# Kernel tuning notes

Measured on AMD Instinct MI355X. Metric: run time of the kernel, lower is better.

Reference implementation:

```python
import jax, jax.numpy as jnp
import numpy as np
from jax import lax

B, C, H, W = 4, 3, 512, 512
PATCH = 64
STRIDE = 32
CHANS = [(3, 32), (32, 32), (32, 64), (64, 64), (64, 64), (64, 32), (32, 32), (32, 2)]


def _conv(x, w, b):
    y = lax.conv_general_dilated(x, w, (1, 1), [(1, 1), (1, 1)],
                                 dimension_numbers=('NCHW', 'OIHW', 'NCHW'))
    return y + b[None, :, None, None]


def _pool(x):  # MaxPool2d(2)
    return lax.reduce_window(x, -jnp.inf, lax.max, (1, 1, 2, 2), (1, 1, 2, 2), 'VALID')


def _up(x):  # Upsample(scale=2, bilinear, align_corners=False) == half-pixel resize
    b, c, h, w = x.shape
    return jax.image.resize(x, (b, c, 2 * h, 2 * w), 'bilinear')


def _flow_net(x, ws, bs):
    r = jax.nn.relu
    h = r(_conv(x, ws[0], bs[0]))
    h = r(_conv(h, ws[1], bs[1]))
    h = _pool(h)
    h = r(_conv(h, ws[2], bs[2]))
    h = r(_conv(h, ws[3], bs[3]))
    h = _pool(h)
    h = _up(h)
    h = r(_conv(h, ws[4], bs[4]))
    h = r(_conv(h, ws[5], bs[5]))
    h = _up(h)
    h = r(_conv(h, ws[6], bs[6]))
    return jnp.tanh(_conv(h, ws[7], bs[7]))  # [B,2,H,W]


def _bilinear_zeros(img, gx, gy):
    # img [C,H,W], gx/gy [N,P,P] in [-1,1]; grid_sample bilinear, zeros padding, align_corners=False
    Hh, Ww = img.shape[1], img.shape[2]
    ix = ((gx + 1.0) * Ww - 1.0) * 0.5
    iy = ((gy + 1.0) * Hh - 1.0) * 0.5
    x0 = jnp.floor(ix)
    y0 = jnp.floor(iy)
    wx1 = ix - x0
    wy1 = iy - y0

    def corner(xi, yi, wgt):
        valid = (xi >= 0) & (xi <= Ww - 1) & (yi >= 0) & (yi <= Hh - 1)
        xc = jnp.clip(xi, 0, Ww - 1).astype(jnp.int32)
        yc = jnp.clip(yi, 0, Hh - 1).astype(jnp.int32)
        return img[:, yc, xc] * (wgt * valid)[None]  # [C,N,P,P]

    return (corner(x0, y0, (1 - wx1) * (1 - wy1))
            + corner(x0 + 1, y0, wx1 * (1 - wy1))
            + corner(x0, y0 + 1, (1 - wx1) * wy1)
            + corner(x0 + 1, y0 + 1, wx1 * wy1))


def _forward(x, ws, bs, temp):
    b, c, h, w = x.shape
    flow = _flow_net(x, ws, bs)  # [B,2,H,W]
    gy, gx = jnp.meshgrid(jnp.linspace(-1.0, 1.0, h), jnp.linspace(-1.0, 1.0, w), indexing='ij')
    base = jnp.stack([gx, gy], axis=-1)  # [H,W,2] (x,y)
    deformed = base[None] + flow.transpose(0, 2, 3, 1) * temp  # [B,H,W,2]
    centers = deformed[:, ::STRIDE, ::STRIDE, :].reshape(b, -1, 2)  # [B,N,2]
    py, px = jnp.meshgrid(jnp.linspace(-1.0, 1.0, PATCH), jnp.linspace(-1.0, 1.0, PATCH), indexing='ij')
    pgx = centers[:, :, None, None, 0] + px[None, None] * (PATCH / w)  # [B,N,P,P]
    pgy = centers[:, :, None, None, 1] + py[None, None] * (PATCH / h)
    patches = jax.vmap(_bilinear_zeros)(x, pgx, pgy)  # [B,C,N,P,P]
    patches = patches.transpose(0, 2, 1, 3, 4)  # [B,N,C,P,P]
    return patches, flow, deformed


def setup_inputs() -> dict:
    key = jax.random.key(0)
    ks = jax.random.split(key, len(CHANS) + 1)
    d = {"x": jax.random.normal(ks[0], (B, C, H, W), jnp.float32)}
    for i, (ci, co) in enumerate(CHANS):
        d[f"w{i}"] = jax.random.normal(ks[i + 1], (co, ci, 3, 3), jnp.float32) * 0.01
        d[f"b{i}"] = jnp.zeros((co,), jnp.float32)
    d["temp"] = jnp.full((1,), 0.1, jnp.float32)
    return d


def reference(x, w0, b0, w1, b1, w2, b2, w3, b3, w4, b4, w5, b5, w6, b6, w7, b7, temp):
    ws = [w0, w1, w2, w3, w4, w5, w6, w7]
    bs = [b0, b1, b2, b3, b4, b5, b6, b7]
    return _forward(x, ws, bs, temp)
```

## Files before the change

kernel.cpp:

```cpp
#include <hip/hip_runtime.h>
#include <hip/hip_bf16.h>

typedef __hip_bfloat16 bf16;
typedef unsigned short ushort_t;
typedef __attribute__((ext_vector_type(8))) short short8;
typedef __attribute__((ext_vector_type(4))) float float4v;

#define BATCH 4
#define HH 512
#define WW 512

__device__ __forceinline__ ushort_t f2bfu(float f) {
  __hip_bfloat16 h = __float2bfloat16(f);
  union { __hip_bfloat16 h; ushort_t u; } c;
  c.h = h;
  return c.u;
}
__device__ __forceinline__ float bfu2f(ushort_t u) {
  return __uint_as_float(((unsigned)u) << 16);
}

__device__ __forceinline__ void dma16(void* lds, const void* g) {
  __builtin_amdgcn_global_load_lds(
      (const __attribute__((address_space(1))) unsigned int*)g,
      (__attribute__((address_space(3))) unsigned int*)lds, 16, 0, 0);
}

struct WP { const float* w[8]; };

__global__ __launch_bounds__(256) void prep_w(WP wp, bf16* __restrict__ dst) {
  const int O[8]   = {32, 32, 64, 64, 64, 32, 32, 2};
  const int I[8]   = {3, 32, 32, 64, 64, 64, 32, 32};
  const int OP[8]  = {32, 32, 64, 64, 64, 32, 32, 16};
  const int IP[8]  = {32, 32, 32, 64, 64, 64, 32, 32};
  const int OFF[8] = {0, 9216, 18432, 36864, 73728, 110592, 129024, 138240};
  int l = blockIdx.y;
  int e = blockIdx.x * 256 + threadIdx.x;
  int n = 9 * OP[l] * IP[l];
  if (e >= n) return;
  int tap = e / (OP[l] * IP[l]);
  int rem = e - tap * OP[l] * IP[l];
  int o = rem / IP[l];
  int i = rem - o * IP[l];
  float v = 0.0f;
  if (o < O[l] && i < I[l]) v = wp.w[l][((o * I[l]) + i) * 9 + tap];
  dst[OFF[l] + e] = __float2bfloat16(v);
}

__global__ __launch_bounds__(256) void pack_x(const float* __restrict__ x,
                                              bf16* __restrict__ xp) {
  int i = blockIdx.x * 256 + threadIdx.x;
  if (i >= BATCH * HH * WW) return;
  int b = i / (HH * WW);
  int px = i - b * (HH * WW);
  union { uint4 v; ushort_t s[8]; } o;
  o.v = make_uint4(0, 0, 0, 0);
  const float* p = x + (long)b * 3 * HH * WW + px;
  o.s[0] = f2bfu(p[0]);
  o.s[1] = f2bfu(p[HH * WW]);
  o.s[2] = f2bfu(p[2 * HH * WW]);
  *(uint4*)&xp[(long)i * 8] = o.v;
}

template <int CIN, int COUT, int COUTR, int ACT, int IN_MODE, int OUT_MODE>
__global__ __launch_bounds__(256) void conv_mfma(
    const void* __restrict__ in_, const bf16* __restrict__ wt,
    const float* __restrict__ bias, void* __restrict__ out_, int H, int W,
    const float* __restrict__ temp, float* __restrict__ def) {
  constexpr int MT = COUT / 16;
  constexpr int CK = 32;
  __shared__ alignas(16) bf16 in_lds[324 * CK];
  __shared__ alignas(16) bf16 w_lds[9 * COUT * CK];

  const int tid = threadIdx.x;
  const int lane = tid & 63;
  const int wid = tid >> 6;
  const int lm = lane & 15;
  const int quad = lane >> 4;
  const int x0 = blockIdx.x * 16;
  const int y0 = blockIdx.y * 16;
  const int b = blockIdx.z;

  float4v acc[MT][4];
#pragma unroll
  for (int mt = 0; mt < MT; ++mt) {
    float4v bv;
    if constexpr (COUTR == COUT) {
      bv = *(const float4v*)(bias + mt * 16 + quad * 4);
    } else {
#pragma unroll
      for (int r = 0; r < 4; ++r) {
        int co = mt * 16 + quad * 4 + r;
        bv[r] = (co < COUTR) ? bias[co] : 0.0f;
      }
    }
#pragma unroll
    for (int nt = 0; nt < 4; ++nt) acc[mt][nt] = bv;
  }

  for (int c0 = 0; c0 < CIN; c0 += CK) {
    if constexpr (IN_MODE == 3) {
      const bf16* in = (const bf16*)in_;
      for (int u = tid; u < 324 * 4; u += 256) {
        int px = u >> 2;
        int seg = u & 3;
        int hy = px / 18, hx = px - hy * 18;
        int gy = y0 - 1 + hy, gx = x0 - 1 + hx;
        uint4 v = make_uint4(0, 0, 0, 0);
        if (seg == 0 && gy >= 0 && gy < H && gx >= 0 && gx < W)
          v = *(const uint4*)(in + (((long)b * H + gy) * W + gx) * 8);
        *(uint4*)&in_lds[px * CK + seg * 8] = v;
      }
    } else if constexpr (IN_MODE == 2) {
      const bf16* in = (const bf16*)in_;
      const int Hs = H >> 1, Ws = W >> 1;
      for (int u = tid; u < 324 * 4; u += 256) {
        int px = u >> 2;
        int seg = u & 3;
        int hy = px / 18, hx = px - hy * 18;
        int gy = y0 - 1 + hy, gx = x0 - 1 + hx;
        uint4 o = make_uint4(0, 0, 0, 0);
        if (gy >= 0 && gy < H && gx >= 0 && gx < W) {
          int ys = (gy >> 1) - ((gy & 1) ? 0 : 1);
          int xs = (gx >> 1) - ((gx & 1) ? 0 : 1);
          float wy = (gy & 1) ? 0.25f : 0.75f;
          float wx = (gx & 1) ? 0.25f : 0.75f;
          int y0c = max(ys, 0), y1c = min(ys + 1, Hs - 1);
          int x0c = max(xs, 0), x1c = min(xs + 1, Ws - 1);
          const bf16* p = in + ((long)b * Hs * Ws) * CIN + c0 + seg * 8;
          union { uint4 v; ushort_t s[8]; } a00, a01, a10, a11, r;
          a00.v = *(const uint4*)(p + ((long)y0c * Ws + x0c) * CIN);
          a01.v = *(const uint4*)(p + ((long)y0c * Ws + x1c) * CIN);
          a10.v = *(const uint4*)(p + ((long)y1c * Ws + x0c) * CIN);
          a11.v = *(const uint4*)(p + ((long)y1c * Ws + x1c) * CIN);
#pragma unroll
          for (int j = 0; j < 8; ++j) {
            float f = (1.0f - wy) * ((1.0f - wx) * bfu2f(a00.s[j]) +
                                     wx * bfu2f(a01.s[j])) +
                      wy * ((1.0f - wx) * bfu2f(a10.s[j]) +
                            wx * bfu2f(a11.s[j]));
            r.s[j] = f2bfu(f);
          }
          o = r.v;
        }
        *(uint4*)&in_lds[px * CK + seg * 8] = o;
      }
    } else {
      const bool interior =
          (x0 >= 1) && (x0 + 16 <= W - 1) && (y0 >= 1) && (y0 + 16 <= H - 1);
      const bf16* in = (const bf16*)in_;
      if (interior) {
        for (int r = wid; r < 18; r += 4) {
          int gy = y0 - 1 + r;
          const bf16* gsrc = in + (((long)b * H + gy) * W + x0) * CIN + c0 +
                             (lane >> 2) * CIN + (lane & 3) * 8;
          dma16(&in_lds[(r * 18 + 1) * CK], gsrc);
        }
        if (tid < 144) {
          int r = tid >> 3;
          int side = (tid >> 2) & 1;
          int seg = tid & 3;
          int gx = side ? (x0 + 16) : (x0 - 1);
          int gy = y0 - 1 + r;
          uint4 v = *(const uint4*)(in + (((long)b * H + gy) * W + gx) * CIN +
                                    c0 + seg * 8);
          *(uint4*)&in_lds[(r * 18 + (side ? 17 : 0)) * CK + seg * 8] = v;
        }
      } else {
        for (int u = tid; u < 324 * 4; u += 256) {
          int px = u >> 2;
          int seg = u & 3;
          int hy = px / 18, hx = px - hy * 18;
          int gy = y0 - 1 + hy, gx = x0 - 1 + hx;
          uint4 v = make_uint4(0, 0, 0, 0);
          if (gy >= 0 && gy < H && gx >= 0 && gx < W)
            v = *(const uint4*)(in + (((long)b * H + gy) * W + gx) * CIN + c0 +
                                seg * 8);
          *(uint4*)&in_lds[px * CK + seg * 8] = v;
        }
      }
    }
    {
      constexpr int WUNITS = 9 * COUT * CK / 8;
      for (int u = tid; u < WUNITS; u += 256) {
        int to = u >> 2;
        int seg = u & 3;
        uint4 v = *(const uint4*)(wt + (long)to * CIN + c0 + seg * 8);
        *(uint4*)&w_lds[to * CK + seg * 8] = v;
      }
    }
    __syncthreads();

#pragma unroll
    for (int tap = 0; tap < 9; ++tap) {
      const int r = tap / 3, s = tap - r * 3;
      short8 afrag[MT], bfrag[4];
#pragma unroll
      for (int mt = 0; mt < MT; ++mt)
        afrag[mt] =
            *(const short8*)&w_lds[(tap * COUT + mt * 16 + lm) * CK + quad * 8];
#pragma unroll
      for (int nt = 0; nt < 4; ++nt) {
        int py = 4 * wid + nt;
        bfrag[nt] =
            *(const short8*)&in_lds[((py + r) * 18 + lm + s) * CK + quad * 8];
      }
#pragma unroll
      for (int mt = 0; mt < MT; ++mt)
#pragma unroll
        for (int nt = 0; nt < 4; ++nt)
          acc[mt][nt] = __builtin_amdgcn_mfma_f32_16x16x32_bf16(
              afrag[mt], bfrag[nt], acc[mt][nt], 0, 0, 0);
    }
    __syncthreads();
  }

  if constexpr (OUT_MODE == 3) {
    bf16* out = (bf16*)out_;
    const int Ho = H >> 1, Wo = W >> 1;
#pragma unroll
    for (int mt = 0; mt < MT; ++mt) {
#pragma unroll
      for (int g = 0; g < 2; ++g) {
        float4v m;
#pragma unroll
        for (int r = 0; r < 4; ++r)
          m[r] = fmaxf(fmaxf(acc[mt][2 * g][r], acc[mt][2 * g + 1][r]), 0.0f);
#pragma unroll
        for (int r = 0; r < 4; ++r) m[r] = fmaxf(m[r], __shfl_xor(m[r], 1, 64));
        if ((lm & 1) == 0) {
          int pyo = (y0 >> 1) + 2 * wid + g;
          int pxo = (x0 >> 1) + (lm >> 1);
          union { uint2 v; ushort_t s[4]; } pk;
#pragma unroll
          for (int r = 0; r < 4; ++r) pk.s[r] = f2bfu(m[r]);
          *(uint2*)&out[(((long)b * Ho + pyo) * Wo + pxo) * COUT + mt * 16 +
                        quad * 4] = pk.v;
        }
      }
    }
  } else {
#pragma unroll
    for (int mt = 0; mt < MT; ++mt) {
#pragma unroll
      for (int nt = 0; nt < 4; ++nt) {
        int gy = y0 + 4 * wid + nt;
        int gx = x0 + lm;
        float4v v = acc[mt][nt];
        if constexpr (OUT_MODE == 0) {
          bf16* out = (bf16*)out_;
          union { uint2 v; ushort_t s[4]; } pk;
#pragma unroll
          for (int r = 0; r < 4; ++r) pk.s[r] = f2bfu(fmaxf(v[r], 0.0f));
          *(uint2*)&out[(((long)b * H + gy) * W + gx) * COUT + mt * 16 +
                        quad * 4] = pk.v;
        } else {
          float* out = (float*)out_;
          if (quad == 0) {
            float fx = tanhf(v[0]);
            float fy = tanhf(v[1]);
            out[(((long)b * 2 + 0) * H + gy) * (long)W + gx] = fx;
            out[(((long)b * 2 + 1) * H + gy) * (long)W + gx] = fy;
            float T = temp[0];
            float2 d;
            d.x = -1.0f + gx * (2.0f / 511.0f) + fx * T;
            d.y = -1.0f + gy * (2.0f / 511.0f) + fy * T;
            *(float2*)&def[(((long)b * H + gy) * W + gx) * 2] = d;
          }
        }
      }
    }
  }
}

__global__ __launch_bounds__(256) void patches_k(const float* __restrict__ x,
                                                 const float* __restrict__ def,
                                                 float* __restrict__ out) {
  int i = blockIdx.x * 256 + threadIdx.x;
  int pj = i & 63;
  int t = i >> 6;
  int pi = t & 63;
  t >>= 6;
  int n = t & 255;
  int b = t >> 8;
  if (b >= BATCH) return;
  int hi = n >> 4, wi = n & 15;
  const float* dptr = def + (((long)b * HH + hi * 32) * WW + wi * 32) * 2;
  float cx = dptr[0], cy = dptr[1];
  float pgx = cx + (-1.0f + pj * (2.0f / 63.0f)) * 0.125f;
  float pgy = cy + (-1.0f + pi * (2.0f / 63.0f)) * 0.125f;
  float ix = ((pgx + 1.0f) * 512.0f - 1.0f) * 0.5f;
  float iy = ((pgy + 1.0f) * 512.0f - 1.0f) * 0.5f;
  float fx0 = floorf(ix), fy0 = floorf(iy);
  float wx1 = ix - fx0, wy1 = iy - fy0;
  int x0 = (int)fx0, y0 = (int)fy0;
  int x1 = x0 + 1, y1 = y0 + 1;
  bool vx0 = (x0 >= 0) && (x0 <= 511), vx1 = (x1 >= 0) && (x1 <= 511);
  bool vy0 = (y0 >= 0) && (y0 <= 511), vy1 = (y1 >= 0) && (y1 <= 511);
  int cx0 = min(max(x0, 0), 511), cx1 = min(max(x1, 0), 511);
  int cy0 = min(max(y0, 0), 511), cy1 = min(max(y1, 0), 511);
  float w00 = (1.0f - wx1) * (1.0f - wy1) * ((vx0 && vy0) ? 1.0f : 0.0f);
  float w01 = wx1 * (1.0f - wy1) * ((vx1 && vy0) ? 1.0f : 0.0f);
  float w10 = (1.0f - wx1) * wy1 * ((vx0 && vy1) ? 1.0f : 0.0f);
  float w11 = wx1 * wy1 * ((vx1 && vy1) ? 1.0f : 0.0f);
#pragma unroll
  for (int c = 0; c < 3; ++c) {
    const float* img = x + ((long)b * 3 + c) * (HH * WW);
    float v = img[cy0 * WW + cx0] * w00 + img[cy0 * WW + cx1] * w01 +
              img[cy1 * WW + cx0] * w10 + img[cy1 * WW + cx1] * w11;
    out[(((long)b * 256 + n) * 3 + c) * 4096 + pi * 64 + pj] = v;
  }
}


extern "C" void kernel_launch(void* const* d_in, const int* in_sizes, int n_in,
                              void* d_out, int out_size, void* d_ws,
                              size_t ws_size, hipStream_t stream) {
  const float* x = (const float*)d_in[0];
  WP wp;
  const float* bs[8];
  for (int i = 0; i < 8; ++i) {
    wp.w[i] = (const float*)d_in[1 + 2 * i];
    bs[i] = (const float*)d_in[2 + 2 * i];
  }
  const float* temp = (const float*)d_in[17];

  float* out = (float*)d_out;
  float* flow = out + 12582912;
  float* def = out + 14680064;

  bf16* wT = (bf16*)d_out;
  const int WOFF[8] = {0, 9216, 18432, 36864, 73728, 110592, 129024, 138240};

  const size_t bufElems = (size_t)BATCH * 512 * 512 * 32;
  bf16* A = (bf16*)d_ws;
  bf16* Bf = A + bufElems;
  bf16* xp = Bf + bufElems;

  prep_w<<<dim3(144, 8), 256, 0, stream>>>(wp, wT);
  {
    int total = BATCH * HH * WW;
    pack_x<<<(total + 255) / 256, 256, 0, stream>>>(x, xp);
  }

  dim3 g512(32, 32, BATCH);
  dim3 g256(16, 16, BATCH);
  dim3 g128(8, 8, BATCH);

  conv_mfma<32, 32, 32, 0, 3, 0>
      <<<g512, 256, 0, stream>>>(xp, wT + WOFF[0], bs[0], A, 512, 512, nullptr, nullptr);
  conv_mfma<32, 32, 32, 0, 0, 3>
      <<<g512, 256, 0, stream>>>(A, wT + WOFF[1], bs[1], Bf, 512, 512, nullptr, nullptr);
  conv_mfma<32, 64, 64, 0, 0, 0>
      <<<g256, 256, 0, stream>>>(Bf, wT + WOFF[2], bs[2], A, 256, 256, nullptr, nullptr);
  conv_mfma<64, 64, 64, 0, 0, 3>
      <<<g256, 256, 0, stream>>>(A, wT + WOFF[3], bs[3], Bf, 256, 256, nullptr, nullptr);
  conv_mfma<64, 64, 64, 0, 2, 0>
      <<<g256, 256, 0, stream>>>(Bf, wT + WOFF[4], bs[4], A, 256, 256, nullptr, nullptr);
  conv_mfma<64, 32, 32, 0, 0, 0>
      <<<g256, 256, 0, stream>>>(A, wT + WOFF[5], bs[5], Bf, 256, 256, nullptr, nullptr);
  conv_mfma<32, 32, 32, 0, 2, 0>
      <<<g512, 256, 0, stream>>>(Bf, wT + WOFF[6], bs[6], A, 512, 512, nullptr, nullptr);
  conv_mfma<32, 16, 2, 1, 0, 2>
      <<<g512, 256, 0, stream>>>(A, wT + WOFF[7], bs[7], flow, 512, 512, temp, def);
  {
    int total = BATCH * 256 * 64 * 64;
    patches_k<<<(total + 255) / 256, 256, 0, stream>>>(x, def, out);
  }
}
```

Baseline: 355.5 us.

## Drop LDS weight staging and make conv tile height a template parameter

Removes the shared-memory copy of the weights. Each wave now reads its A fragments straight from global memory, relying on cache hits for the small weight tensor. It also adds an NT template parameter so the 32-channel conv layers use 16x32 output tiles. Taller tiles reuse the halo better and halve the block count. The trade-off is more live accumulator registers and global-latency weight loads inside the MFMA loop, which could lower occupancy or stall the inner loop.

```diff
diff --git a/kernel.cpp b/kernel.cpp
--- a/kernel.cpp
+++ b/kernel.cpp
@@ -62,15 +62,17 @@
   *(uint4*)&xp[(long)i * 8] = o.v;
 }
 
-template <int CIN, int COUT, int COUTR, int ACT, int IN_MODE, int OUT_MODE>
+template <int CIN, int COUT, int COUTR, int NT, int ACT, int IN_MODE,
+          int OUT_MODE>
 __global__ __launch_bounds__(256) void conv_mfma(
     const void* __restrict__ in_, const bf16* __restrict__ wt,
     const float* __restrict__ bias, void* __restrict__ out_, int H, int W,
     const float* __restrict__ temp, float* __restrict__ def) {
   constexpr int MT = COUT / 16;
   constexpr int CK = 32;
-  __shared__ alignas(16) bf16 in_lds[324 * CK];
-  __shared__ alignas(16) bf16 w_lds[9 * COUT * CK];
+  constexpr int TH = 4 * NT;
+  constexpr int HR = TH + 2;
+  __shared__ alignas(16) bf16 in_lds[HR * 18 * CK];
 
   const int tid = threadIdx.x;
   const int lane = tid & 63;
@@ -78,10 +80,10 @@
   const int lm = lane & 15;
   const int quad = lane >> 4;
   const int x0 = blockIdx.x * 16;
-  const int y0 = blockIdx.y * 16;
+  const int y0 = blockIdx.y * TH;
   const int b = blockIdx.z;
 
-  float4v acc[MT][4];
+  float4v acc[MT][NT];
 #pragma unroll
   for (int mt = 0; mt < MT; ++mt) {
     float4v bv;
@@ -95,13 +97,13 @@
       }
     }
 #pragma unroll
-    for (int nt = 0; nt < 4; ++nt) acc[mt][nt] = bv;
+    for (int nt = 0; nt < NT; ++nt) acc[mt][nt] = bv;
   }
 
   for (int c0 = 0; c0 < CIN; c0 += CK) {
     if constexpr (IN_MODE == 3) {
       const bf16* in = (const bf16*)in_;
-      for (int u = tid; u < 324 * 4; u += 256) {
+      for (int u = tid; u < HR * 18 * 4; u += 256) {
         int px = u >> 2;
         int seg = u & 3;
         int hy = px / 18, hx = px - hy * 18;
@@ -114,7 +116,7 @@
     } else if constexpr (IN_MODE == 2) {
       const bf16* in = (const bf16*)in_;
       const int Hs = H >> 1, Ws = W >> 1;
-      for (int u = tid; u < 324 * 4; u += 256) {
+      for (int u = tid; u < HR * 18 * 4; u += 256) {
         int px = u >> 2;
         int seg = u & 3;
         int hy = px / 18, hx = px - hy * 18;
@@ -147,19 +149,19 @@
       }
     } else {
       const bool interior =
-          (x0 >= 1) && (x0 + 16 <= W - 1) && (y0 >= 1) && (y0 + 16 <= H - 1);
+          (x0 >= 1) && (x0 + 16 <= W - 1) && (y0 >= 1) && (y0 + TH <= H - 1);
       const bf16* in = (const bf16*)in_;
       if (interior) {
-        for (int r = wid; r < 18; r += 4) {
+        for (int r = wid; r < HR; r += 4) {
           int gy = y0 - 1 + r;
           const bf16* gsrc = in + (((long)b * H + gy) * W + x0) * CIN + c0 +
                              (lane >> 2) * CIN + (lane & 3) * 8;
           dma16(&in_lds[(r * 18 + 1) * CK], gsrc);
         }
-        if (tid < 144) {
-          int r = tid >> 3;
-          int side = (tid >> 2) & 1;
-          int seg = tid & 3;
+        for (int u = tid; u < 8 * HR; u += 256) {
+          int r = u >> 3;
+          int side = (u >> 2) & 1;
+          int seg = u & 3;
           int gx = side ? (x0 + 16) : (x0 - 1);
           int gy = y0 - 1 + r;
           uint4 v = *(const uint4*)(in + (((long)b * H + gy) * W + gx) * CIN +
@@ -167,7 +169,7 @@
           *(uint4*)&in_lds[(r * 18 + (side ? 17 : 0)) * CK + seg * 8] = v;
         }
       } else {
-        for (int u = tid; u < 324 * 4; u += 256) {
+        for (int u = tid; u < HR * 18 * 4; u += 256) {
           int px = u >> 2;
           int seg = u & 3;
           int hy = px / 18, hx = px - hy * 18;
@@ -180,35 +182,26 @@
         }
       }
     }
-    {
-      constexpr int WUNITS = 9 * COUT * CK / 8;
-      for (int u = tid; u < WUNITS; u += 256) {
-        int to = u >> 2;
-        int seg = u & 3;
-        uint4 v = *(const uint4*)(wt + (long)to * CIN + c0 + seg * 8);
-        *(uint4*)&w_lds[to * CK + seg * 8] = v;
-      }
-    }
     __syncthreads();
 
 #pragma unroll
     for (int tap = 0; tap < 9; ++tap) {
       const int r = tap / 3, s = tap - r * 3;
-      short8 afrag[MT], bfrag[4];
+      short8 afrag[MT], bfrag[NT];
 #pragma unroll
       for (int mt = 0; mt < MT; ++mt)
-        afrag[mt] =
-            *(const short8*)&w_lds[(tap * COUT + mt * 16 + lm) * CK + quad * 8];
-#pragma unroll
-      for (int nt = 0; nt < 4; ++nt) {
-        int py = 4 * wid + nt;
+        afrag[mt] = *(const short8*)&wt[((long)tap * COUT + mt * 16 + lm) * CIN +
+                                        c0 + quad * 8];
+#pragma unroll
+      for (int nt = 0; nt < NT; ++nt) {
+        int py = NT * wid + nt;
         bfrag[nt] =
             *(const short8*)&in_lds[((py + r) * 18 + lm + s) * CK + quad * 8];
       }
 #pragma unroll
       for (int mt = 0; mt < MT; ++mt)
 #pragma unroll
-        for (int nt = 0; nt < 4; ++nt)
+        for (int nt = 0; nt < NT; ++nt)
           acc[mt][nt] = __builtin_amdgcn_mfma_f32_16x16x32_bf16(
               afrag[mt], bfrag[nt], acc[mt][nt], 0, 0, 0);
     }
@@ -221,7 +214,7 @@
 #pragma unroll
     for (int mt = 0; mt < MT; ++mt) {
 #pragma unroll
-      for (int g = 0; g < 2; ++g) {
+      for (int g = 0; g < NT / 2; ++g) {
         float4v m;
 #pragma unroll
         for (int r = 0; r < 4; ++r)
@@ -229,7 +222,7 @@
 #pragma unroll
         for (int r = 0; r < 4; ++r) m[r] = fmaxf(m[r], __shfl_xor(m[r], 1, 64));
         if ((lm & 1) == 0) {
-          int pyo = (y0 >> 1) + 2 * wid + g;
+          int pyo = (y0 >> 1) + (NT / 2) * wid + g;
           int pxo = (x0 >> 1) + (lm >> 1);
           union { uint2 v; ushort_t s[4]; } pk;
 #pragma unroll
@@ -243,8 +236,8 @@
 #pragma unroll
     for (int mt = 0; mt < MT; ++mt) {
 #pragma unroll
-      for (int nt = 0; nt < 4; ++nt) {
-        int gy = y0 + 4 * wid + nt;
+      for (int nt = 0; nt < NT; ++nt) {
+        int gy = y0 + NT * wid + nt;
         int gx = x0 + lm;
         float4v v = acc[mt][nt];
         if constexpr (OUT_MODE == 0) {
@@ -343,26 +336,26 @@
     pack_x<<<(total + 255) / 256, 256, 0, stream>>>(x, xp);
   }
 
-  dim3 g512(32, 32, BATCH);
+  dim3 g512t(32, 16, BATCH);
+  dim3 g256t(16, 8, BATCH);
   dim3 g256(16, 16, BATCH);
-  dim3 g128(8, 8, BATCH);
-
-  conv_mfma<32, 32, 32, 0, 3, 0>
-      <<<g512, 256, 0, stream>>>(xp, wT + WOFF[0], bs[0], A, 512, 512, nullptr, nullptr);
-  conv_mfma<32, 32, 32, 0, 0, 3>
-      <<<g512, 256, 0, stream>>>(A, wT + WOFF[1], bs[1], Bf, 512, 512, nullptr, nullptr);
-  conv_mfma<32, 64, 64, 0, 0, 0>
+
+  conv_mfma<32, 32, 32, 8, 0, 3, 0>
+      <<<g512t, 256, 0, stream>>>(xp, wT + WOFF[0], bs[0], A, 512, 512, nullptr, nullptr);
+  conv_mfma<32, 32, 32, 8, 0, 0, 3>
+      <<<g512t, 256, 0, stream>>>(A, wT + WOFF[1], bs[1], Bf, 512, 512, nullptr, nullptr);
+  conv_mfma<32, 64, 64, 4, 0, 0, 0>
       <<<g256, 256, 0, stream>>>(Bf, wT + WOFF[2], bs[2], A, 256, 256, nullptr, nullptr);
-  conv_mfma<64, 64, 64, 0, 0, 3>
+  conv_mfma<64, 64, 64, 4, 0, 0, 3>
       <<<g256, 256, 0, stream>>>(A, wT + WOFF[3], bs[3], Bf, 256, 256, nullptr, nullptr);
-  conv_mfma<64, 64, 64, 0, 2, 0>
+  conv_mfma<64, 64, 64, 4, 0, 2, 0>
       <<<g256, 256, 0, stream>>>(Bf, wT + WOFF[4], bs[4], A, 256, 256, nullptr, nullptr);
-  conv_mfma<64, 32, 32, 0, 0, 0>
-      <<<g256, 256, 0, stream>>>(A, wT + WOFF[5], bs[5], Bf, 256, 256, nullptr, nullptr);
-  conv_mfma<32, 32, 32, 0, 2, 0>
-      <<<g512, 256, 0, stream>>>(Bf, wT + WOFF[6], bs[6], A, 512, 512, nullptr, nullptr);
-  conv_mfma<32, 16, 2, 1, 0, 2>
-      <<<g512, 256, 0, stream>>>(A, wT + WOFF[7], bs[7], flow, 512, 512, temp, def);
+  conv_mfma<64, 32, 32, 8, 0, 0, 0>
+      <<<g256t, 256, 0, stream>>>(A, wT + WOFF[5], bs[5], Bf, 256, 256, nullptr, nullptr);
+  conv_mfma<32, 32, 32, 8, 0, 2, 0>
+      <<<g512t, 256, 0, stream>>>(Bf, wT + WOFF[6], bs[6], A, 512, 512, nullptr, nullptr);
+  conv_mfma<32, 16, 2, 8, 1, 0, 2>
+      <<<g512t, 256, 0, stream>>>(A, wT + WOFF[7], bs[7], flow, 512, 512, temp, def);
   {
     int total = BATCH * 256 * 64 * 64;
     patches_k<<<(total + 255) / 256, 256, 0, stream>>>(x, def, out);
```

Result: slower. 429.8 us (+20.9%).

## Fold bilinear upsample into conv6 via polyphase weights; keep weights in registers

Applied to the files above, without the earlier changes.

Replaces the upsample-then-3x3-conv at full resolution with a polyphase convolution on the low-resolution input. Per-phase 3x3 weights are precomputed by folding the bilinear 0.75/0.25 interpolation into conv6's weights. The main kernel clamps at the low-res edges, so a separate scalar kernel recomputes the border ring exactly. Single-chunk convolutions (CIN=32) also load their weight fragments directly into registers instead of staging them through LDS. This removes the per-pixel interpolation work and weight LDS traffic, in exchange for higher register pressure and an extra small launch.

```diff
diff --git a/kernel.cpp b/kernel.cpp
--- a/kernel.cpp
+++ b/kernel.cpp
@@ -47,6 +47,28 @@
   dst[OFF[l] + e] = __float2bfloat16(v);
 }
 
+__global__ __launch_bounds__(256) void prep_w6p(const float* __restrict__ w6,
+                                                bf16* __restrict__ wP) {
+  int e = blockIdx.x * 256 + threadIdx.x;
+  if (e >= 4 * 9 * 32 * 32) return;
+  int i = e & 31;
+  int o = (e >> 5) & 31;
+  int tap = (e >> 10) % 9;
+  int phase = (e >> 10) / 9;
+  int j = tap / 3, k = tap % 3;
+  int phi = phase >> 1, psi = phase & 1;
+  const float R[2][3][3] = {
+      {{0.75f, 0.25f, 0.0f}, {0.25f, 0.75f, 0.0f}, {0.0f, 0.75f, 0.25f}},
+      {{0.25f, 0.75f, 0.0f}, {0.0f, 0.75f, 0.25f}, {0.0f, 0.25f, 0.75f}}};
+  float acc = 0.0f;
+#pragma unroll
+  for (int r = 0; r < 3; ++r)
+#pragma unroll
+    for (int s = 0; s < 3; ++s)
+      acc += w6[((o * 32 + i) * 3 + r) * 3 + s] * R[phi][r][j] * R[psi][s][k];
+  wP[e] = __float2bfloat16(acc);
+}
+
 __global__ __launch_bounds__(256) void pack_x(const float* __restrict__ x,
                                               bf16* __restrict__ xp) {
   int i = blockIdx.x * 256 + threadIdx.x;
@@ -62,7 +84,8 @@
   *(uint4*)&xp[(long)i * 8] = o.v;
 }
 
-template <int CIN, int COUT, int COUTR, int ACT, int IN_MODE, int OUT_MODE>
+template <int CIN, int COUT, int COUTR, int ACT, int IN_MODE, int OUT_MODE,
+          bool WREG>
 __global__ __launch_bounds__(256) void conv_mfma(
     const void* __restrict__ in_, const bf16* __restrict__ wt,
     const float* __restrict__ bias, void* __restrict__ out_, int H, int W,
@@ -70,7 +93,7 @@
   constexpr int MT = COUT / 16;
   constexpr int CK = 32;
   __shared__ alignas(16) bf16 in_lds[324 * CK];
-  __shared__ alignas(16) bf16 w_lds[9 * COUT * CK];
+  __shared__ alignas(16) bf16 w_lds[WREG ? 16 : 9 * COUT * CK];
 
   const int tid = threadIdx.x;
   const int lane = tid & 63;
@@ -80,6 +103,17 @@
   const int x0 = blockIdx.x * 16;
   const int y0 = blockIdx.y * 16;
   const int b = blockIdx.z;
+
+  short8 wreg[WREG ? 9 : 1][MT];
+  if constexpr (WREG) {
+    static_assert(CIN == CK, "WREG requires single K chunk");
+#pragma unroll
+    for (int tap = 0; tap < 9; ++tap)
+#pragma unroll
+      for (int mt = 0; mt < MT; ++mt)
+        wreg[tap][mt] = *(const short8*)&wt[((long)tap * COUT + mt * 16 + lm) *
+                                               CIN + quad * 8];
+  }
 
   float4v acc[MT][4];
 #pragma unroll
@@ -156,10 +190,10 @@
                              (lane >> 2) * CIN + (lane & 3) * 8;
           dma16(&in_lds[(r * 18 + 1) * CK], gsrc);
         }
-        if (tid < 144) {
-          int r = tid >> 3;
-          int side = (tid >> 2) & 1;
-          int seg = tid & 3;
+        for (int u = tid; u < 144; u += 256) {
+          int r = u >> 3;
+          int side = (u >> 2) & 1;
+          int seg = u & 3;
           int gx = side ? (x0 + 16) : (x0 - 1);
           int gy = y0 - 1 + r;
           uint4 v = *(const uint4*)(in + (((long)b * H + gy) * W + gx) * CIN +
@@ -180,7 +214,7 @@
         }
       }
     }
-    {
+    if constexpr (!WREG) {
       constexpr int WUNITS = 9 * COUT * CK / 8;
       for (int u = tid; u < WUNITS; u += 256) {
         int to = u >> 2;
@@ -196,9 +230,13 @@
       const int r = tap / 3, s = tap - r * 3;
       short8 afrag[MT], bfrag[4];
 #pragma unroll
-      for (int mt = 0; mt < MT; ++mt)
-        afrag[mt] =
-            *(const short8*)&w_lds[(tap * COUT + mt * 16 + lm) * CK + quad * 8];
+      for (int mt = 0; mt < MT; ++mt) {
+        if constexpr (WREG)
+          afrag[mt] = wreg[tap][mt];
+        else
+          afrag[mt] = *(const short8*)&w_lds[(tap * COUT + mt * 16 + lm) * CK +
+                                             quad * 8];
+      }
 #pragma unroll
       for (int nt = 0; nt < 4; ++nt) {
         int py = 4 * wid + nt;
@@ -271,6 +309,176 @@
       }
     }
   }
+}
+
+__global__ __launch_bounds__(256) void conv_up_phase(
+    const bf16* __restrict__ in,
+    const bf16* __restrict__ wP,
+    const float* __restrict__ bias, bf16* __restrict__ out, int Hs, int Ws) {
+  constexpr int CK = 32;
+  constexpr int MT = 2;
+  __shared__ alignas(16) bf16 in_lds[324 * CK];
+
+  const int tid = threadIdx.x;
+  const int lane = tid & 63;
+  const int wid = tid >> 6;
+  const int lm = lane & 15;
+  const int quad = lane >> 4;
+  const int x0 = blockIdx.x * 16;
+  const int y0 = blockIdx.y * 16;
+  const int b = blockIdx.z;
+  const int H = 2 * Hs, W = 2 * Ws;
+
+  const bool interior =
+      (x0 >= 1) && (x0 + 16 <= Ws - 1) && (y0 >= 1) && (y0 + 16 <= Hs - 1);
+  if (interior) {
+    for (int r = wid; r < 18; r += 4) {
+      int gy = y0 - 1 + r;
+      const bf16* gsrc = in + (((long)b * Hs + gy) * Ws + x0) * CK +
+                         (lane >> 2) * CK + (lane & 3) * 8;
+      dma16(&in_lds[(r * 18 + 1) * CK], gsrc);
+    }
+    for (int u = tid; u < 144; u += 256) {
+      int r = u >> 3;
+      int side = (u >> 2) & 1;
+      int seg = u & 3;
+      int gx = side ? (x0 + 16) : (x0 - 1);
+      int gy = y0 - 1 + r;
+      uint4 v = *(const uint4*)(in + (((long)b * Hs + gy) * Ws + gx) * CK +
+                                seg * 8);
+      *(uint4*)&in_lds[(r * 18 + (side ? 17 : 0)) * CK + seg * 8] = v;
+    }
+  } else {
+    for (int u = tid; u < 324 * 4; u += 256) {
+      int px = u >> 2;
+      int seg = u & 3;
+      int hy = px / 18, hx = px - hy * 18;
+      int gy = min(max(y0 - 1 + hy, 0), Hs - 1);
+      int gx = min(max(x0 - 1 + hx, 0), Ws - 1);
+      uint4 v =
+          *(const uint4*)(in + (((long)b * Hs + gy) * Ws + gx) * CK + seg * 8);
+      *(uint4*)&in_lds[px * CK + seg * 8] = v;
+    }
+  }
+  __syncthreads();
+
+  for (int phase = 0; phase < 4; ++phase) {
+    const int phi = phase >> 1, psi = phase & 1;
+    short8 wreg[9][MT];
+#pragma unroll
+    for (int tap = 0; tap < 9; ++tap)
+#pragma unroll
+      for (int mt = 0; mt < MT; ++mt)
+        wreg[tap][mt] = *(const short8*)&wP[(((long)phase * 9 + tap) * 32 +
+                                            mt * 16 + lm) * 32 + quad * 8];
+    float4v acc[MT][4];
+#pragma unroll
+    for (int mt = 0; mt < MT; ++mt) {
+      float4v bv = *(const float4v*)(bias + mt * 16 + quad * 4);
+#pragma unroll
+      for (int nt = 0; nt < 4; ++nt) acc[mt][nt] = bv;
+    }
+#pragma unroll
+    for (int tap = 0; tap < 9; ++tap) {
+      const int r = tap / 3, s = tap - r * 3;
+      short8 bfrag[4];
+#pragma unroll
+      for (int nt = 0; nt < 4; ++nt) {
+        int py = 4 * wid + nt;
+        bfrag[nt] =
+            *(const short8*)&in_lds[((py + r) * 18 + lm + s) * CK + quad * 8];
+      }
+#pragma unroll
+      for (int mt = 0; mt < MT; ++mt)
+#pragma unroll
+        for (int nt = 0; nt < 4; ++nt)
+          acc[mt][nt] = __builtin_amdgcn_mfma_f32_16x16x32_bf16(
+              wreg[tap][mt], bfrag[nt], acc[mt][nt], 0, 0, 0);
+    }
+#pragma unroll
+    for (int mt = 0; mt < MT; ++mt) {
+#pragma unroll
+      for (int nt = 0; nt < 4; ++nt) {
+        int y = y0 + 4 * wid + nt;
+        int x = x0 + lm;
+        int Y = 2 * y + phi;
+        int X = 2 * x + psi;
+        if (Y >= 1 && Y <= H - 2 && X >= 1 && X <= W - 2) {
+          union { uint2 v; ushort_t s[4]; } pk;
+#pragma unroll
+          for (int r = 0; r < 4; ++r)
+            pk.s[r] = f2bfu(fmaxf(acc[mt][nt][r], 0.0f));
+          *(uint2*)&out[(((long)b * H + Y) * W + X) * 32 + mt * 16 + quad * 4] =
+              pk.v;
+        }
+      }
+    }
+  }
+}
+
+__global__ __launch_bounds__(256) void conv_ring(
+    const bf16* __restrict__ V,
+    const bf16* __restrict__ w6,
+    const float* __restrict__ bias, bf16* __restrict__ out) {
+  int t = blockIdx.x * 256 + threadIdx.x;
+  if (t >= BATCH * 2044 * 4) return;
+  int seg = t & 3;
+  t >>= 2;
+  int m = t % 2044;
+  int b = t / 2044;
+  int Y, X;
+  if (m < 512) { Y = 0; X = m; }
+  else if (m < 1024) { Y = 511; X = m - 512; }
+  else if (m < 1534) { Y = m - 1024 + 1; X = 0; }
+  else { Y = m - 1534 + 1; X = 511; }
+  float acc[8];
+#pragma unroll
+  for (int j = 0; j < 8; ++j) acc[j] = bias[seg * 8 + j];
+#pragma unroll
+  for (int r = 0; r < 3; ++r) {
+    int q = Y - 1 + r;
+    if (q < 0 || q > 511) continue;
+    int ys = (q >> 1) - ((q & 1) ? 0 : 1);
+    float wy = (q & 1) ? 0.25f : 0.75f;
+    int y0c = max(ys, 0), y1c = min(ys + 1, 255);
+#pragma unroll
+    for (int s = 0; s < 3; ++s) {
+      int p = X - 1 + s;
+      if (p < 0 || p > 511) continue;
+      int xs = (p >> 1) - ((p & 1) ? 0 : 1);
+      float wx = (p & 1) ? 0.25f : 0.75f;
+      int x0c = max(xs, 0), x1c = min(xs + 1, 255);
+      int tap = r * 3 + s;
+      for (int is = 0; is < 4; ++is) {
+        union { uint4 v; ushort_t u[8]; } a00, a01, a10, a11;
+        const bf16* base = V + ((long)b * 256 * 256) * 32 + is * 8;
+        a00.v = *(const uint4*)(base + ((long)y0c * 256 + x0c) * 32);
+        a01.v = *(const uint4*)(base + ((long)y0c * 256 + x1c) * 32);
+        a10.v = *(const uint4*)(base + ((long)y1c * 256 + x0c) * 32);
+        a11.v = *(const uint4*)(base + ((long)y1c * 256 + x1c) * 32);
+        float u8[8];
+#pragma unroll
+        for (int j = 0; j < 8; ++j)
+          u8[j] = (1.0f - wy) * ((1.0f - wx) * bfu2f(a00.u[j]) +
+                                 wx * bfu2f(a01.u[j])) +
+                  wy * ((1.0f - wx) * bfu2f(a10.u[j]) + wx * bfu2f(a11.u[j]));
+#pragma unroll
+        for (int co = 0; co < 8; ++co) {
+          union { uint4 v; ushort_t u[8]; } wv;
+          wv.v = *(const uint4*)(w6 + ((long)tap * 32 + seg * 8 + co) * 32 +
+                                 is * 8);
+          float a = acc[co];
+#pragma unroll
+          for (int j = 0; j < 8; ++j) a += u8[j] * bfu2f(wv.u[j]);
+          acc[co] = a;
+        }
+      }
+    }
+  }
+  union { uint4 v; ushort_t u[8]; } o;
+#pragma unroll
+  for (int j = 0; j < 8; ++j) o.u[j] = f2bfu(fmaxf(acc[j], 0.0f));
+  *(uint4*)&out[(((long)b * 512 + Y) * 512 + X) * 32 + seg * 8] = o.v;
 }
 
 __global__ __launch_bounds__(256) void patches_k(const float* __restrict__ x,
@@ -336,8 +544,10 @@
   bf16* A = (bf16*)d_ws;
   bf16* Bf = A + bufElems;
   bf16* xp = Bf + bufElems;
+  bf16* wP6 = xp + (size_t)BATCH * 512 * 512 * 8;
 
   prep_w<<<dim3(144, 8), 256, 0, stream>>>(wp, wT);
+  prep_w6p<<<144, 256, 0, stream>>>(wp.w[6], wP6);
   {
     int total = BATCH * HH * WW;
     pack_x<<<(total + 255) / 256, 256, 0, stream>>>(x, xp);
@@ -345,23 +555,25 @@
 
   dim3 g512(32, 32, BATCH);
   dim3 g256(16, 16, BATCH);
-  dim3 g128(8, 8, BATCH);
-
-  conv_mfma<32, 32, 32, 0, 3, 0>
+
+  conv_mfma<32, 32, 32, 0, 3, 0, true>
       <<<g512, 256, 0, stream>>>(xp, wT + WOFF[0], bs[0], A, 512, 512, nullptr, nullptr);
-  conv_mfma<32, 32, 32, 0, 0, 3>
+  conv_mfma<32, 32, 32, 0, 0, 3, true>
       <<<g512, 256, 0, stream>>>(A, wT + WOFF[1], bs[1], Bf, 512, 512, nullptr, nullptr);
-  conv_mfma<32, 64, 64, 0, 0, 0>
+  conv_mfma<32, 64, 64, 0, 0, 0, false>
       <<<g256, 256, 0, stream>>>(Bf, wT + WOFF[2], bs[2], A, 256, 256, nullptr, nullptr);
-  conv_mfma<64, 64, 64, 0, 0, 3>
+  conv_mfma<64, 64, 64, 0, 0, 3, false>
       <<<g256, 256, 0, stream>>>(A, wT + WOFF[3], bs[3], Bf, 256, 256, nullptr, nullptr);
-  conv_mfma<64, 64, 64, 0, 2, 0>
+  conv_mfma<64, 64, 64, 0, 2, 0, false>
       <<<g256, 256, 0, stream>>>(Bf, wT + WOFF[4], bs[4], A, 256, 256, nullptr, nullptr);
-  conv_mfma<64, 32, 32, 0, 0, 0>
+  conv_mfma<64, 32, 32, 0, 0, 0, false>
       <<<g256, 256, 0, stream>>>(A, wT + WOFF[5], bs[5], Bf, 256, 256, nullptr, nullptr);
-  conv_mfma<32, 32, 32, 0, 2, 0>
-      <<<g512, 256, 0, stream>>>(Bf, wT + WOFF[6], bs[6], A, 512, 512, nullptr, nullptr);
-  conv_mfma<32, 16, 2, 1, 0, 2>
+  conv_up_phase<<<g256, 256, 0, stream>>>(Bf, wP6, bs[6], A, 256, 256);
+  {
+    int total = BATCH * 2044 * 4;
+    conv_ring<<<(total + 255) / 256, 256, 0, stream>>>(Bf, wT + WOFF[6], bs[6], A);
+  }
+  conv_mfma<32, 16, 2, 1, 0, 2, true>
       <<<g512, 256, 0, stream>>>(A, wT + WOFF[7], bs[7], flow, 512, 512, temp, def);
   {
     int total = BATCH * 256 * 64 * 64;
```

After: 399.4 us. +12.3%, slower.
